# Optimization experiments

Measured on AMD Instinct MI355X. Metric: run time of the kernel, lower is better.

## Reference

```python
import jax, jax.numpy as jnp
import numpy as np

N_NODES = 100000
N_EDGES = 1600000
D = 128
N_GRAPHS = 1024
N_LAYERS = 3
BN_EPS = 1e-5


def setup_inputs() -> dict:
    key = jax.random.key(0)
    ks = jax.random.split(key, 12)
    x = jax.random.normal(ks[0], (N_NODES, D), dtype=jnp.float32)
    edge_index = jax.random.randint(ks[1], (2, N_EDGES), 0, N_NODES, dtype=jnp.int32)
    batch = jnp.sort(jax.random.randint(ks[2], (N_NODES,), 0, N_GRAPHS, dtype=jnp.int32))
    scale = 1.0 / np.sqrt(D)
    W1 = jax.random.uniform(ks[3], (D, D), jnp.float32, -scale, scale)
    b1 = jax.random.uniform(ks[4], (D,), jnp.float32, -scale, scale)
    W2 = jax.random.uniform(ks[5], (D, D), jnp.float32, -scale, scale)
    b2 = jax.random.uniform(ks[6], (D,), jnp.float32, -scale, scale)
    W3 = jax.random.uniform(ks[7], (D, D), jnp.float32, -scale, scale)
    b3 = jax.random.uniform(ks[8], (D,), jnp.float32, -scale, scale)
    eps = jnp.zeros((N_LAYERS,), jnp.float32)          # GINConv train_eps init = 0
    gamma = jnp.ones((N_LAYERS, D), jnp.float32)       # BatchNorm1d weight
    beta = jnp.zeros((N_LAYERS, D), jnp.float32)       # BatchNorm1d bias
    return {"x": x, "edge_index": edge_index, "batch": batch,
            "W1": W1, "b1": b1, "W2": W2, "b2": b2, "W3": W3, "b3": b3,
            "eps": eps, "gamma": gamma, "beta": beta}


def _gin_layer(h, src, dst, W, b, eps_i, g, bt):
    # scatter-add neighbor aggregation: sum_{j in N(i)} h_j
    agg = jax.ops.segment_sum(h[src], dst, num_segments=N_NODES)  # [N, D]
    h = (1.0 + eps_i) * h + agg
    h = h @ W.T + b                                   # Linear
    mean = jnp.mean(h, axis=0)                        # BatchNorm1d (training, biased var)
    var = jnp.var(h, axis=0)
    h = (h - mean) * jax.lax.rsqrt(var + BN_EPS) * g + bt
    return jax.nn.relu(h)


def reference(x, edge_index, batch, W1, b1, W2, b2, W3, b3, eps, gamma, beta):
    src, dst = edge_index[0], edge_index[1]
    h = x
    for i, (W, b) in enumerate([(W1, b1), (W2, b2), (W3, b3)]):
        h = _gin_layer(h, src, dst, W, b, eps[i], gamma[i], beta[i])
    # global mean pool over graphs
    sums = jax.ops.segment_sum(h, batch, num_segments=N_GRAPHS)             # [G, D]
    counts = jax.ops.segment_sum(jnp.ones((h.shape[0],), h.dtype), batch,
                                 num_segments=N_GRAPHS)                      # [G]
    return sums / jnp.maximum(counts, 1.0)[:, None]
```

## Files before the change

kernel.cpp:

```cpp
#include <hip/hip_runtime.h>

#define N_NODES 100000
#define N_PAD 100032
#define N_EDGES 1600000
#define DIM 128
#define N_GRAPHS 1024

#define SCAN_BLOCK 256
#define SCAN_NB ((N_NODES + SCAN_BLOCK - 1) / SCAN_BLOCK)

#define NPART 8
#define PART_SZ 12500

typedef __bf16 bf16x8 __attribute__((ext_vector_type(8)));
typedef float f32x4 __attribute__((ext_vector_type(4)));

__device__ __forceinline__ unsigned short f2bf(float f) {
    unsigned u = __builtin_bit_cast(unsigned, f);
    u += 0x7fffu + ((u >> 16) & 1u);
    return (unsigned short)(u >> 16);
}
__device__ __forceinline__ unsigned pk2(float a, float b) {
    return (unsigned)f2bf(a) | ((unsigned)f2bf(b) << 16);
}
__device__ __forceinline__ float bf2f(unsigned short s) {
    return __builtin_bit_cast(float, (unsigned)s << 16);
}
__device__ __forceinline__ void dec2(unsigned p, float& lo, float& hi) {
    lo = __builtin_bit_cast(float, p << 16);
    hi = __builtin_bit_cast(float, p & 0xffff0000u);
}


__global__ __launch_bounds__(256) void hist_part_kernel(const int* __restrict__ dst,
                                                        int* __restrict__ deg) {
    int p = blockIdx.x & (NPART - 1);
    int bgrp = blockIdx.x >> 3;
    int nb = gridDim.x >> 3;
    int tid = bgrp * blockDim.x + threadIdx.x;
    int nthreads = nb * blockDim.x;
    const int NE4 = N_EDGES / 4;
    for (int i = tid; i < NE4; i += nthreads) {
        int4 d4 = ((const int4*)dst)[i];
        if (d4.x / PART_SZ == p) atomicAdd(&deg[d4.x], 1);
        if (d4.y / PART_SZ == p) atomicAdd(&deg[d4.y], 1);
        if (d4.z / PART_SZ == p) atomicAdd(&deg[d4.z], 1);
        if (d4.w / PART_SZ == p) atomicAdd(&deg[d4.w], 1);
    }
}

__global__ __launch_bounds__(256) void fill_part_kernel(const int* __restrict__ src,
                                                        const int* __restrict__ dst,
                                                        int* __restrict__ cursor,
                                                        int* __restrict__ csr) {
    int p = blockIdx.x & (NPART - 1);
    int bgrp = blockIdx.x >> 3;
    int nb = gridDim.x >> 3;
    int tid = bgrp * blockDim.x + threadIdx.x;
    int nthreads = nb * blockDim.x;
    const int NE4 = N_EDGES / 4;
    for (int i = tid; i < NE4; i += nthreads) {
        int4 d4 = ((const int4*)dst)[i];
        int4 s4 = ((const int4*)src)[i];
        if (d4.x / PART_SZ == p) csr[atomicAdd(&cursor[d4.x], 1)] = s4.x;
        if (d4.y / PART_SZ == p) csr[atomicAdd(&cursor[d4.y], 1)] = s4.y;
        if (d4.z / PART_SZ == p) csr[atomicAdd(&cursor[d4.z], 1)] = s4.z;
        if (d4.w / PART_SZ == p) csr[atomicAdd(&cursor[d4.w], 1)] = s4.w;
    }
}


__global__ __launch_bounds__(SCAN_BLOCK) void scan_partial_kernel(const int* __restrict__ deg,
                                                                  int* __restrict__ partials) {
    __shared__ int red[SCAN_BLOCK / 64];
    int i = blockIdx.x * SCAN_BLOCK + threadIdx.x;
    int v = (i < N_NODES) ? deg[i] : 0;
    for (int o = 32; o > 0; o >>= 1) v += __shfl_down(v, o, 64);
    if ((threadIdx.x & 63) == 0) red[threadIdx.x >> 6] = v;
    __syncthreads();
    if (threadIdx.x == 0) {
        int s = 0;
#pragma unroll
        for (int w = 0; w < SCAN_BLOCK / 64; ++w) s += red[w];
        partials[blockIdx.x] = s;
    }
}

__global__ __launch_bounds__(512) void scan_partials_kernel(int* __restrict__ partials,
                                                            int* __restrict__ off) {
    __shared__ int sm[512];
    int t = threadIdx.x;
    int v = (t < SCAN_NB) ? partials[t] : 0;
    sm[t] = v;
    __syncthreads();
    for (int o = 1; o < 512; o <<= 1) {
        int u = (t >= o) ? sm[t - o] : 0;
        __syncthreads();
        sm[t] += u;
        __syncthreads();
    }
    if (t < SCAN_NB) partials[t] = sm[t] - v;
    if (t == 0) off[N_NODES] = sm[511];
}

__global__ __launch_bounds__(SCAN_BLOCK) void scan_scatter_kernel(const int* __restrict__ deg,
                                                                  const int* __restrict__ partials,
                                                                  int* __restrict__ off,
                                                                  int* __restrict__ cursor) {
    __shared__ int sm[SCAN_BLOCK];
    int t = threadIdx.x;
    int i = blockIdx.x * SCAN_BLOCK + t;
    int v = (i < N_NODES) ? deg[i] : 0;
    sm[t] = v;
    __syncthreads();
    for (int o = 1; o < SCAN_BLOCK; o <<= 1) {
        int u = (t >= o) ? sm[t - o] : 0;
        __syncthreads();
        sm[t] += u;
        __syncthreads();
    }
    if (i < N_NODES) {
        int r = partials[blockIdx.x] + sm[t] - v;
        off[i] = r;
        cursor[i] = r;
    }
}


__global__ __launch_bounds__(64) void wprep_kernel(const float* __restrict__ W1,
                                                   const float* __restrict__ W2,
                                                   const float* __restrict__ W3,
                                                   uint4* __restrict__ wb4) {
    int b = blockIdx.x;
    int l = b >> 5;
    int nt = (b >> 2) & 7;
    int kk = b & 3;
    int lane = threadIdx.x;
    const float* W = (l == 0) ? W1 : (l == 1) ? W2 : W3;
    int row = nt * 16 + (lane & 15);
    int cb = kk * 32 + (lane >> 4) * 8;
    const float* g = W + row * DIM + cb;
    float4 f0 = *(const float4*)g;
    float4 f1 = *(const float4*)(g + 4);
    uint4 o;
    o.x = pk2(f0.x, f0.y);
    o.y = pk2(f0.z, f0.w);
    o.z = pk2(f1.x, f1.y);
    o.w = pk2(f1.z, f1.w);
    wb4[(size_t)b * 64 + lane] = o;
}


__global__ __launch_bounds__(256) void xconv_kernel(const float* __restrict__ x,
                                                    unsigned short* __restrict__ xb) {
    int i = blockIdx.x * blockDim.x + threadIdx.x;
    int stride = gridDim.x * blockDim.x;
    const int TOT = N_PAD * DIM / 8;
    for (; i < TOT; i += stride) {
        int row = i >> 4;
        int ks = i & 15;
        uint4 o = {0, 0, 0, 0};
        if (row < N_NODES) {
            const float* g = x + (size_t)row * DIM + ks * 8;
            float4 f0 = *(const float4*)g;
            float4 f1 = *(const float4*)(g + 4);
            o.x = pk2(f0.x, f0.y);
            o.y = pk2(f0.z, f0.w);
            o.z = pk2(f1.x, f1.y);
            o.w = pk2(f1.z, f1.w);
        }
        ((uint4*)xb)[i] = o;
    }
}


template <bool BN>
__global__ __launch_bounds__(256) void agg_gemm_kernel(const unsigned short* __restrict__ hin,
                                                       const int* __restrict__ off,
                                                       const int* __restrict__ csr,
                                                       const float* __restrict__ eps_arr, int layer,
                                                       const float* __restrict__ bnsc,
                                                       const float* __restrict__ bnsh,
                                                       const uint4* __restrict__ wb4,
                                                       unsigned short* __restrict__ y,
                                                       float* __restrict__ colsum,
                                                       float* __restrict__ colsumsq) {
    __shared__ unsigned short tile[64 * DIM];
    __shared__ float sstat[4][DIM];
    __shared__ float sstatq[4][DIM];
    int tid = threadIdx.x;
    int row0 = blockIdx.x * 64;
    int grp = tid >> 4;
    int lane = tid & 15;
    float se = 1.0f + eps_arr[layer];
    float sc[8], sh[8];
    if (BN) {
        float4 c0 = *(const float4*)(bnsc + lane * 8);
        float4 c1 = *(const float4*)(bnsc + lane * 8 + 4);
        float4 h0 = *(const float4*)(bnsh + lane * 8);
        float4 h1 = *(const float4*)(bnsh + lane * 8 + 4);
        sc[0] = c0.x; sc[1] = c0.y; sc[2] = c0.z; sc[3] = c0.w;
        sc[4] = c1.x; sc[5] = c1.y; sc[6] = c1.z; sc[7] = c1.w;
        sh[0] = h0.x; sh[1] = h0.y; sh[2] = h0.z; sh[3] = h0.w;
        sh[4] = h1.x; sh[5] = h1.y; sh[6] = h1.z; sh[7] = h1.w;
    }
    const uint4* base = (const uint4*)hin + lane;

#pragma unroll 1
    for (int r4 = 0; r4 < 4; ++r4) {
        int trow = grp * 4 + r4;
        int row = row0 + trow;
        float a[8] = {0.f, 0.f, 0.f, 0.f, 0.f, 0.f, 0.f, 0.f};
        if (row < N_NODES) {
            {
                uint4 pv = base[(size_t)row * (DIM / 8)];
                float v[8];
                dec2(pv.x, v[0], v[1]); dec2(pv.y, v[2], v[3]);
                dec2(pv.z, v[4], v[5]); dec2(pv.w, v[6], v[7]);
#pragma unroll
                for (int j = 0; j < 8; ++j) {
                    if (BN) v[j] = fmaxf(fmaf(v[j], sc[j], sh[j]), 0.f);
                    a[j] = se * v[j];
                }
            }
            int k = off[row], e = off[row + 1];
            for (; k + 3 < e; k += 4) {
                int s0 = csr[k], s1 = csr[k + 1], s2 = csr[k + 2], s3 = csr[k + 3];
                uint4 p0 = base[(size_t)s0 * (DIM / 8)];
                uint4 p1 = base[(size_t)s1 * (DIM / 8)];
                uint4 p2 = base[(size_t)s2 * (DIM / 8)];
                uint4 p3 = base[(size_t)s3 * (DIM / 8)];
                float v0[8], v1[8], v2[8], v3[8];
                dec2(p0.x, v0[0], v0[1]); dec2(p0.y, v0[2], v0[3]);
                dec2(p0.z, v0[4], v0[5]); dec2(p0.w, v0[6], v0[7]);
                dec2(p1.x, v1[0], v1[1]); dec2(p1.y, v1[2], v1[3]);
                dec2(p1.z, v1[4], v1[5]); dec2(p1.w, v1[6], v1[7]);
                dec2(p2.x, v2[0], v2[1]); dec2(p2.y, v2[2], v2[3]);
                dec2(p2.z, v2[4], v2[5]); dec2(p2.w, v2[6], v2[7]);
                dec2(p3.x, v3[0], v3[1]); dec2(p3.y, v3[2], v3[3]);
                dec2(p3.z, v3[4], v3[5]); dec2(p3.w, v3[6], v3[7]);
#pragma unroll
                for (int j = 0; j < 8; ++j) {
                    if (BN) {
                        v0[j] = fmaxf(fmaf(v0[j], sc[j], sh[j]), 0.f);
                        v1[j] = fmaxf(fmaf(v1[j], sc[j], sh[j]), 0.f);
                        v2[j] = fmaxf(fmaf(v2[j], sc[j], sh[j]), 0.f);
                        v3[j] = fmaxf(fmaf(v3[j], sc[j], sh[j]), 0.f);
                    }
                    a[j] += (v0[j] + v1[j]) + (v2[j] + v3[j]);
                }
            }
            for (; k < e; ++k) {
                int s0 = csr[k];
                uint4 p0 = base[(size_t)s0 * (DIM / 8)];
                float v0[8];
                dec2(p0.x, v0[0], v0[1]); dec2(p0.y, v0[2], v0[3]);
                dec2(p0.z, v0[4], v0[5]); dec2(p0.w, v0[6], v0[7]);
#pragma unroll
                for (int j = 0; j < 8; ++j) {
                    if (BN) v0[j] = fmaxf(fmaf(v0[j], sc[j], sh[j]), 0.f);
                    a[j] += v0[j];
                }
            }
        }
        uint4 pw;
        pw.x = pk2(a[0], a[1]);
        pw.y = pk2(a[2], a[3]);
        pw.z = pk2(a[4], a[5]);
        pw.w = pk2(a[6], a[7]);
        int byte = (trow * 256 + lane * 16) ^ ((trow & 7) << 4);
        *(uint4*)((char*)tile + byte) = pw;
    }
    __syncthreads();

    int w = tid >> 6;
    int l = tid & 63;
    int lr = l & 15;
    int lg = l >> 4;
    bf16x8 a[4];
#pragma unroll
    for (int kk = 0; kk < 4; ++kk) {
        int row = w * 16 + lr;
        int byte = (row * 256 + kk * 64 + lg * 16) ^ ((row & 7) << 4);
        a[kk] = __builtin_bit_cast(bf16x8, *(uint4*)((char*)tile + byte));
    }

#pragma unroll
    for (int nt = 0; nt < 8; ++nt) {
        f32x4 acc = {0.0f, 0.0f, 0.0f, 0.0f};
#pragma unroll
        for (int kk = 0; kk < 4; ++kk) {
            bf16x8 b = __builtin_bit_cast(bf16x8, wb4[(nt * 4 + kk) * 64 + l]);
            acc = __builtin_amdgcn_mfma_f32_16x16x32_bf16(a[kk], b, acc, 0, 0, 0);
        }
        int col = nt * 16 + lr;
        size_t base2 = (size_t)(row0 + w * 16 + lg * 4) * DIM + col;
        y[base2] = f2bf(acc[0]);
        y[base2 + DIM] = f2bf(acc[1]);
        y[base2 + 2 * DIM] = f2bf(acc[2]);
        y[base2 + 3 * DIM] = f2bf(acc[3]);
        float s = acc[0] + acc[1] + acc[2] + acc[3];
        float q = acc[0] * acc[0] + acc[1] * acc[1] + acc[2] * acc[2] + acc[3] * acc[3];
        s += __shfl_xor(s, 16);
        s += __shfl_xor(s, 32);
        q += __shfl_xor(q, 16);
        q += __shfl_xor(q, 32);
        if (lg == 0) {
            sstat[w][col] = s;
            sstatq[w][col] = q;
        }
    }
    __syncthreads();
    if (tid < DIM) {
        float s = sstat[0][tid] + sstat[1][tid] + sstat[2][tid] + sstat[3][tid];
        float q = sstatq[0][tid] + sstatq[1][tid] + sstatq[2][tid] + sstatq[3][tid];
        atomicAdd(&colsum[tid], s);
        atomicAdd(&colsumsq[tid], q);
    }
}


__global__ void bnfin_kernel(float* __restrict__ colsum, float* __restrict__ colsumsq,
                             const float* __restrict__ gamma, const float* __restrict__ beta,
                             float* __restrict__ scale, float* __restrict__ shift) {
    int d = threadIdx.x;
    float m = colsum[d] * (1.0f / N_NODES);
    float v = colsumsq[d] * (1.0f / N_NODES) - m * m;
    float sc = gamma[d] * rsqrtf(v + 1e-5f);
    scale[d] = sc;
    shift[d] = beta[d] - m * sc;
    colsum[d] = 0.0f;
    colsumsq[d] = 0.0f;
}


__global__ __launch_bounds__(128) void pool_kernel(const unsigned short* __restrict__ y,
                                                   const int* __restrict__ batch,
                                                   const float* __restrict__ bnsc,
                                                   const float* __restrict__ bnsh,
                                                   float* __restrict__ out) {
    int gph = blockIdx.x;
    int d = threadIdx.x;
    int lo = 0, hi = N_NODES;
    while (lo < hi) {
        int mid = (lo + hi) >> 1;
        if (batch[mid] < gph) lo = mid + 1; else hi = mid;
    }
    int start = lo;
    hi = N_NODES;
    while (lo < hi) {
        int mid = (lo + hi) >> 1;
        if (batch[mid] < gph + 1) lo = mid + 1; else hi = mid;
    }
    int end = lo;
    float sc = bnsc[d], sh = bnsh[d];
    float s = 0.0f;
    for (int n = start; n < end; ++n) {
        float v = bf2f(y[(size_t)n * DIM + d]);
        s += fmaxf(fmaf(v, sc, sh), 0.0f);
    }
    out[gph * DIM + d] = s / fmaxf((float)(end - start), 1.0f);
}


extern "C" void kernel_launch(void* const* d_in, const int* in_sizes, int n_in,
                              void* d_out, int out_size, void* d_ws, size_t ws_size,
                              hipStream_t stream) {
    const float* x = (const float*)d_in[0];
    const int* ei = (const int*)d_in[1];
    const int* batch = (const int*)d_in[2];
    const float* Wp[3] = {(const float*)d_in[3], (const float*)d_in[5], (const float*)d_in[7]};
    const float* eps = (const float*)d_in[9];
    const float* gamma = (const float*)d_in[10];
    const float* beta = (const float*)d_in[11];
    float* out = (float*)d_out;

    char* ws = (char*)d_ws;
    size_t o = 0;
    auto alloc = [&](size_t bytes) {
        void* p = ws + o;
        o = (o + bytes + 255) & ~(size_t)255;
        return p;
    };
    int* deg = (int*)alloc(N_NODES * sizeof(int));
    int* off = (int*)alloc((N_NODES + 1) * sizeof(int));
    int* cursor = (int*)alloc(N_NODES * sizeof(int));
    int* partials = (int*)alloc(SCAN_NB * sizeof(int));
    int* csr = (int*)alloc(N_EDGES * sizeof(int));
    uint4* wb4 = (uint4*)alloc(3 * 8 * 4 * 64 * 16);
    float* colsum = (float*)alloc(DIM * sizeof(float));
    float* colsumsq = (float*)alloc(DIM * sizeof(float));
    float* bnsc = (float*)alloc(DIM * sizeof(float));
    float* bnsh = (float*)alloc(DIM * sizeof(float));
    unsigned short* xb = (unsigned short*)alloc((size_t)N_PAD * DIM * 2);
    unsigned short* y0 = (unsigned short*)alloc((size_t)N_PAD * DIM * 2);
    unsigned short* y1 = (unsigned short*)alloc((size_t)N_PAD * DIM * 2);

    hipMemsetAsync(deg, 0, N_NODES * sizeof(int), stream);
    hipMemsetAsync(colsum, 0, DIM * sizeof(float), stream);
    hipMemsetAsync(colsumsq, 0, DIM * sizeof(float), stream);

    hist_part_kernel<<<1024, 256, 0, stream>>>(ei + N_EDGES, deg);
    scan_partial_kernel<<<SCAN_NB, SCAN_BLOCK, 0, stream>>>(deg, partials);
    scan_partials_kernel<<<1, 512, 0, stream>>>(partials, off);
    scan_scatter_kernel<<<SCAN_NB, SCAN_BLOCK, 0, stream>>>(deg, partials, off, cursor);
    fill_part_kernel<<<1024, 256, 0, stream>>>(ei, ei + N_EDGES, cursor, csr);
    wprep_kernel<<<96, 64, 0, stream>>>(Wp[0], Wp[1], Wp[2], wb4);
    xconv_kernel<<<2048, 256, 0, stream>>>(x, xb);

    const int NBLK = N_PAD / 64;
    agg_gemm_kernel<false><<<NBLK, 256, 0, stream>>>(xb, off, csr, eps, 0, bnsc, bnsh,
                                                     wb4, y0, colsum, colsumsq);
    bnfin_kernel<<<1, DIM, 0, stream>>>(colsum, colsumsq, gamma, beta, bnsc, bnsh);
    agg_gemm_kernel<true><<<NBLK, 256, 0, stream>>>(y0, off, csr, eps, 1, bnsc, bnsh,
                                                    wb4 + 2048, y1, colsum, colsumsq);
    bnfin_kernel<<<1, DIM, 0, stream>>>(colsum, colsumsq, gamma + DIM, beta + DIM, bnsc, bnsh);
    agg_gemm_kernel<true><<<NBLK, 256, 0, stream>>>(y1, off, csr, eps, 2, bnsc, bnsh,
                                                    wb4 + 4096, y0, colsum, colsumsq);
    bnfin_kernel<<<1, DIM, 0, stream>>>(colsum, colsumsq, gamma + 2 * DIM, beta + 2 * DIM, bnsc, bnsh);
    pool_kernel<<<N_GRAPHS, DIM, 0, stream>>>(y0, batch, bnsc, bnsh, out);
}
```

Before: 614.9 us.

## Fold BN finalize into consumers, unroll gather by 8, widen edge and pool loops

Removes the three single-block bnfin kernels. Each consumer kernel (the next agg_gemm or pool) now recomputes BN scale and shift from per-layer column-sum buffers, which cuts launch overhead and serialization points. The neighbor-gather loop is unrolled to 8 outstanding row loads for more memory-level parallelism. The histogram and CSR fill kernels read 8 edges per iteration with a doubled grid, and pool uses 4 independent accumulators. The cost is redundant per-thread rsqrt work, higher register pressure in the gather loop, and 3x larger stat buffers that are zeroed up front.

```diff
diff --git a/kernel.cpp b/kernel.cpp
--- a/kernel.cpp
+++ b/kernel.cpp
@@ -29,6 +29,20 @@
 __device__ __forceinline__ void dec2(unsigned p, float& lo, float& hi) {
     lo = __builtin_bit_cast(float, p << 16);
     hi = __builtin_bit_cast(float, p & 0xffff0000u);
+}
+
+template <bool BN>
+__device__ __forceinline__ void acc8(uint4 p, float* a, const float* sc, const float* sh) {
+    float v[8];
+    dec2(p.x, v[0], v[1]);
+    dec2(p.y, v[2], v[3]);
+    dec2(p.z, v[4], v[5]);
+    dec2(p.w, v[6], v[7]);
+#pragma unroll
+    for (int j = 0; j < 8; ++j) {
+        float t = BN ? fmaxf(fmaf(v[j], sc[j], sh[j]), 0.f) : v[j];
+        a[j] += t;
+    }
 }
 
 
@@ -39,13 +53,18 @@
     int nb = gridDim.x >> 3;
     int tid = bgrp * blockDim.x + threadIdx.x;
     int nthreads = nb * blockDim.x;
-    const int NE4 = N_EDGES / 4;
-    for (int i = tid; i < NE4; i += nthreads) {
-        int4 d4 = ((const int4*)dst)[i];
-        if (d4.x / PART_SZ == p) atomicAdd(&deg[d4.x], 1);
-        if (d4.y / PART_SZ == p) atomicAdd(&deg[d4.y], 1);
-        if (d4.z / PART_SZ == p) atomicAdd(&deg[d4.z], 1);
-        if (d4.w / PART_SZ == p) atomicAdd(&deg[d4.w], 1);
+    const int NE8 = N_EDGES / 8;
+    for (int i = tid; i < NE8; i += nthreads) {
+        int4 a = ((const int4*)dst)[2 * i];
+        int4 b = ((const int4*)dst)[2 * i + 1];
+        if (a.x / PART_SZ == p) atomicAdd(&deg[a.x], 1);
+        if (a.y / PART_SZ == p) atomicAdd(&deg[a.y], 1);
+        if (a.z / PART_SZ == p) atomicAdd(&deg[a.z], 1);
+        if (a.w / PART_SZ == p) atomicAdd(&deg[a.w], 1);
+        if (b.x / PART_SZ == p) atomicAdd(&deg[b.x], 1);
+        if (b.y / PART_SZ == p) atomicAdd(&deg[b.y], 1);
+        if (b.z / PART_SZ == p) atomicAdd(&deg[b.z], 1);
+        if (b.w / PART_SZ == p) atomicAdd(&deg[b.w], 1);
     }
 }
 
@@ -58,14 +77,20 @@
     int nb = gridDim.x >> 3;
     int tid = bgrp * blockDim.x + threadIdx.x;
     int nthreads = nb * blockDim.x;
-    const int NE4 = N_EDGES / 4;
-    for (int i = tid; i < NE4; i += nthreads) {
-        int4 d4 = ((const int4*)dst)[i];
-        int4 s4 = ((const int4*)src)[i];
-        if (d4.x / PART_SZ == p) csr[atomicAdd(&cursor[d4.x], 1)] = s4.x;
-        if (d4.y / PART_SZ == p) csr[atomicAdd(&cursor[d4.y], 1)] = s4.y;
-        if (d4.z / PART_SZ == p) csr[atomicAdd(&cursor[d4.z], 1)] = s4.z;
-        if (d4.w / PART_SZ == p) csr[atomicAdd(&cursor[d4.w], 1)] = s4.w;
+    const int NE8 = N_EDGES / 8;
+    for (int i = tid; i < NE8; i += nthreads) {
+        int4 da = ((const int4*)dst)[2 * i];
+        int4 db = ((const int4*)dst)[2 * i + 1];
+        int4 sa = ((const int4*)src)[2 * i];
+        int4 sb = ((const int4*)src)[2 * i + 1];
+        if (da.x / PART_SZ == p) csr[atomicAdd(&cursor[da.x], 1)] = sa.x;
+        if (da.y / PART_SZ == p) csr[atomicAdd(&cursor[da.y], 1)] = sa.y;
+        if (da.z / PART_SZ == p) csr[atomicAdd(&cursor[da.z], 1)] = sa.z;
+        if (da.w / PART_SZ == p) csr[atomicAdd(&cursor[da.w], 1)] = sa.w;
+        if (db.x / PART_SZ == p) csr[atomicAdd(&cursor[db.x], 1)] = sb.x;
+        if (db.y / PART_SZ == p) csr[atomicAdd(&cursor[db.y], 1)] = sb.y;
+        if (db.z / PART_SZ == p) csr[atomicAdd(&cursor[db.z], 1)] = sb.z;
+        if (db.w / PART_SZ == p) csr[atomicAdd(&cursor[db.w], 1)] = sb.w;
     }
 }
 
@@ -179,12 +204,14 @@
                                                        const int* __restrict__ off,
                                                        const int* __restrict__ csr,
                                                        const float* __restrict__ eps_arr, int layer,
-                                                       const float* __restrict__ bnsc,
-                                                       const float* __restrict__ bnsh,
+                                                       const float* __restrict__ csum_prev,
+                                                       const float* __restrict__ csq_prev,
+                                                       const float* __restrict__ gamma_prev,
+                                                       const float* __restrict__ beta_prev,
                                                        const uint4* __restrict__ wb4,
                                                        unsigned short* __restrict__ y,
-                                                       float* __restrict__ colsum,
-                                                       float* __restrict__ colsumsq) {
+                                                       float* __restrict__ csum_out,
+                                                       float* __restrict__ csq_out) {
     __shared__ unsigned short tile[64 * DIM];
     __shared__ float sstat[4][DIM];
     __shared__ float sstatq[4][DIM];
@@ -195,16 +222,18 @@
     float se = 1.0f + eps_arr[layer];
     float sc[8], sh[8];
     if (BN) {
-        float4 c0 = *(const float4*)(bnsc + lane * 8);
-        float4 c1 = *(const float4*)(bnsc + lane * 8 + 4);
-        float4 h0 = *(const float4*)(bnsh + lane * 8);
-        float4 h1 = *(const float4*)(bnsh + lane * 8 + 4);
-        sc[0] = c0.x; sc[1] = c0.y; sc[2] = c0.z; sc[3] = c0.w;
-        sc[4] = c1.x; sc[5] = c1.y; sc[6] = c1.z; sc[7] = c1.w;
-        sh[0] = h0.x; sh[1] = h0.y; sh[2] = h0.z; sh[3] = h0.w;
-        sh[4] = h1.x; sh[5] = h1.y; sh[6] = h1.z; sh[7] = h1.w;
+#pragma unroll
+        for (int j = 0; j < 8; ++j) {
+            int d = lane * 8 + j;
+            float m = csum_prev[d] * (1.0f / N_NODES);
+            float var = csq_prev[d] * (1.0f / N_NODES) - m * m;
+            float s = gamma_prev[d] * rsqrtf(var + 1e-5f);
+            sc[j] = s;
+            sh[j] = beta_prev[d] - m * s;
+        }
     }
     const uint4* base = (const uint4*)hin + lane;
+    const size_t RS = DIM / 8;
 
 #pragma unroll 1
     for (int r4 = 0; r4 < 4; ++r4) {
@@ -213,54 +242,52 @@
         float a[8] = {0.f, 0.f, 0.f, 0.f, 0.f, 0.f, 0.f, 0.f};
         if (row < N_NODES) {
             {
-                uint4 pv = base[(size_t)row * (DIM / 8)];
+                uint4 pv = base[(size_t)row * RS];
                 float v[8];
                 dec2(pv.x, v[0], v[1]); dec2(pv.y, v[2], v[3]);
                 dec2(pv.z, v[4], v[5]); dec2(pv.w, v[6], v[7]);
 #pragma unroll
                 for (int j = 0; j < 8; ++j) {
-                    if (BN) v[j] = fmaxf(fmaf(v[j], sc[j], sh[j]), 0.f);
-                    a[j] = se * v[j];
+                    float t = BN ? fmaxf(fmaf(v[j], sc[j], sh[j]), 0.f) : v[j];
+                    a[j] = se * t;
                 }
             }
             int k = off[row], e = off[row + 1];
-            for (; k + 3 < e; k += 4) {
+            for (; k + 7 < e; k += 8) {
                 int s0 = csr[k], s1 = csr[k + 1], s2 = csr[k + 2], s3 = csr[k + 3];
-                uint4 p0 = base[(size_t)s0 * (DIM / 8)];
-                uint4 p1 = base[(size_t)s1 * (DIM / 8)];
-                uint4 p2 = base[(size_t)s2 * (DIM / 8)];
-                uint4 p3 = base[(size_t)s3 * (DIM / 8)];
-                float v0[8], v1[8], v2[8], v3[8];
-                dec2(p0.x, v0[0], v0[1]); dec2(p0.y, v0[2], v0[3]);
-                dec2(p0.z, v0[4], v0[5]); dec2(p0.w, v0[6], v0[7]);
-                dec2(p1.x, v1[0], v1[1]); dec2(p1.y, v1[2], v1[3]);
-                dec2(p1.z, v1[4], v1[5]); dec2(p1.w, v1[6], v1[7]);
-                dec2(p2.x, v2[0], v2[1]); dec2(p2.y, v2[2], v2[3]);
-                dec2(p2.z, v2[4], v2[5]); dec2(p2.w, v2[6], v2[7]);
-                dec2(p3.x, v3[0], v3[1]); dec2(p3.y, v3[2], v3[3]);
-                dec2(p3.z, v3[4], v3[5]); dec2(p3.w, v3[6], v3[7]);
-#pragma unroll
-                for (int j = 0; j < 8; ++j) {
-                    if (BN) {
-                        v0[j] = fmaxf(fmaf(v0[j], sc[j], sh[j]), 0.f);
-                        v1[j] = fmaxf(fmaf(v1[j], sc[j], sh[j]), 0.f);
-                        v2[j] = fmaxf(fmaf(v2[j], sc[j], sh[j]), 0.f);
-                        v3[j] = fmaxf(fmaf(v3[j], sc[j], sh[j]), 0.f);
-                    }
-                    a[j] += (v0[j] + v1[j]) + (v2[j] + v3[j]);
-                }
+                int s4 = csr[k + 4], s5 = csr[k + 5], s6 = csr[k + 6], s7 = csr[k + 7];
+                uint4 p0 = base[(size_t)s0 * RS];
+                uint4 p1 = base[(size_t)s1 * RS];
+                uint4 p2 = base[(size_t)s2 * RS];
+                uint4 p3 = base[(size_t)s3 * RS];
+                uint4 p4 = base[(size_t)s4 * RS];
+                uint4 p5 = base[(size_t)s5 * RS];
+                uint4 p6 = base[(size_t)s6 * RS];
+                uint4 p7 = base[(size_t)s7 * RS];
+                acc8<BN>(p0, a, sc, sh);
+                acc8<BN>(p1, a, sc, sh);
+                acc8<BN>(p2, a, sc, sh);
+                acc8<BN>(p3, a, sc, sh);
+                acc8<BN>(p4, a, sc, sh);
+                acc8<BN>(p5, a, sc, sh);
+                acc8<BN>(p6, a, sc, sh);
+                acc8<BN>(p7, a, sc, sh);
+            }
+            if (k + 3 < e) {
+                int s0 = csr[k], s1 = csr[k + 1], s2 = csr[k + 2], s3 = csr[k + 3];
+                uint4 p0 = base[(size_t)s0 * RS];
+                uint4 p1 = base[(size_t)s1 * RS];
+                uint4 p2 = base[(size_t)s2 * RS];
+                uint4 p3 = base[(size_t)s3 * RS];
+                acc8<BN>(p0, a, sc, sh);
+                acc8<BN>(p1, a, sc, sh);
+                acc8<BN>(p2, a, sc, sh);
+                acc8<BN>(p3, a, sc, sh);
+                k += 4;
             }
             for (; k < e; ++k) {
-                int s0 = csr[k];
-                uint4 p0 = base[(size_t)s0 * (DIM / 8)];
-                float v0[8];
-                dec2(p0.x, v0[0], v0[1]); dec2(p0.y, v0[2], v0[3]);
-                dec2(p0.z, v0[4], v0[5]); dec2(p0.w, v0[6], v0[7]);
-#pragma unroll
-                for (int j = 0; j < 8; ++j) {
-                    if (BN) v0[j] = fmaxf(fmaf(v0[j], sc[j], sh[j]), 0.f);
-                    a[j] += v0[j];
-                }
+                uint4 p0 = base[(size_t)csr[k] * RS];
+                acc8<BN>(p0, a, sc, sh);
             }
         }
         uint4 pw;
@@ -314,33 +341,25 @@
     if (tid < DIM) {
         float s = sstat[0][tid] + sstat[1][tid] + sstat[2][tid] + sstat[3][tid];
         float q = sstatq[0][tid] + sstatq[1][tid] + sstatq[2][tid] + sstatq[3][tid];
-        atomicAdd(&colsum[tid], s);
-        atomicAdd(&colsumsq[tid], q);
-    }
-}
-
-
-__global__ void bnfin_kernel(float* __restrict__ colsum, float* __restrict__ colsumsq,
-                             const float* __restrict__ gamma, const float* __restrict__ beta,
-                             float* __restrict__ scale, float* __restrict__ shift) {
-    int d = threadIdx.x;
-    float m = colsum[d] * (1.0f / N_NODES);
-    float v = colsumsq[d] * (1.0f / N_NODES) - m * m;
-    float sc = gamma[d] * rsqrtf(v + 1e-5f);
-    scale[d] = sc;
-    shift[d] = beta[d] - m * sc;
-    colsum[d] = 0.0f;
-    colsumsq[d] = 0.0f;
+        atomicAdd(&csum_out[tid], s);
+        atomicAdd(&csq_out[tid], q);
+    }
 }
 
 
 __global__ __launch_bounds__(128) void pool_kernel(const unsigned short* __restrict__ y,
                                                    const int* __restrict__ batch,
-                                                   const float* __restrict__ bnsc,
-                                                   const float* __restrict__ bnsh,
+                                                   const float* __restrict__ csum,
+                                                   const float* __restrict__ csq,
+                                                   const float* __restrict__ gamma,
+                                                   const float* __restrict__ beta,
                                                    float* __restrict__ out) {
     int gph = blockIdx.x;
     int d = threadIdx.x;
+    float m = csum[d] * (1.0f / N_NODES);
+    float var = csq[d] * (1.0f / N_NODES) - m * m;
+    float sc = gamma[d] * rsqrtf(var + 1e-5f);
+    float sh = beta[d] - m * sc;
     int lo = 0, hi = N_NODES;
     while (lo < hi) {
         int mid = (lo + hi) >> 1;
@@ -353,12 +372,23 @@
         if (batch[mid] < gph + 1) lo = mid + 1; else hi = mid;
     }
     int end = lo;
-    float sc = bnsc[d], sh = bnsh[d];
-    float s = 0.0f;
-    for (int n = start; n < end; ++n) {
+    float s0 = 0.f, s1 = 0.f, s2 = 0.f, s3 = 0.f;
+    int n = start;
+    for (; n + 3 < end; n += 4) {
+        float v0 = bf2f(y[(size_t)n * DIM + d]);
+        float v1 = bf2f(y[(size_t)(n + 1) * DIM + d]);
+        float v2 = bf2f(y[(size_t)(n + 2) * DIM + d]);
+        float v3 = bf2f(y[(size_t)(n + 3) * DIM + d]);
+        s0 += fmaxf(fmaf(v0, sc, sh), 0.0f);
+        s1 += fmaxf(fmaf(v1, sc, sh), 0.0f);
+        s2 += fmaxf(fmaf(v2, sc, sh), 0.0f);
+        s3 += fmaxf(fmaf(v3, sc, sh), 0.0f);
+    }
+    for (; n < end; ++n) {
         float v = bf2f(y[(size_t)n * DIM + d]);
-        s += fmaxf(fmaf(v, sc, sh), 0.0f);
-    }
+        s0 += fmaxf(fmaf(v, sc, sh), 0.0f);
+    }
+    float s = (s0 + s1) + (s2 + s3);
     out[gph * DIM + d] = s / fmaxf((float)(end - start), 1.0f);
 }
 
@@ -388,35 +418,34 @@
     int* partials = (int*)alloc(SCAN_NB * sizeof(int));
     int* csr = (int*)alloc(N_EDGES * sizeof(int));
     uint4* wb4 = (uint4*)alloc(3 * 8 * 4 * 64 * 16);
-    float* colsum = (float*)alloc(DIM * sizeof(float));
-    float* colsumsq = (float*)alloc(DIM * sizeof(float));
-    float* bnsc = (float*)alloc(DIM * sizeof(float));
-    float* bnsh = (float*)alloc(DIM * sizeof(float));
+    float* csums = (float*)alloc(3 * DIM * sizeof(float));
+    float* csqs = (float*)alloc(3 * DIM * sizeof(float));
     unsigned short* xb = (unsigned short*)alloc((size_t)N_PAD * DIM * 2);
     unsigned short* y0 = (unsigned short*)alloc((size_t)N_PAD * DIM * 2);
     unsigned short* y1 = (unsigned short*)alloc((size_t)N_PAD * DIM * 2);
 
     hipMemsetAsync(deg, 0, N_NODES * sizeof(int), stream);
-    hipMemsetAsync(colsum, 0, DIM * sizeof(float), stream);
-    hipMemsetAsync(colsumsq, 0, DIM * sizeof(float), stream);
-
-    hist_part_kernel<<<1024, 256, 0, stream>>>(ei + N_EDGES, deg);
+    hipMemsetAsync(csums, 0, 3 * DIM * sizeof(float), stream);
+    hipMemsetAsync(csqs, 0, 3 * DIM * sizeof(float), stream);
+
+    hist_part_kernel<<<2048, 256, 0, stream>>>(ei + N_EDGES, deg);
     scan_partial_kernel<<<SCAN_NB, SCAN_BLOCK, 0, stream>>>(deg, partials);
     scan_partials_kernel<<<1, 512, 0, stream>>>(partials, off);
     scan_scatter_kernel<<<SCAN_NB, SCAN_BLOCK, 0, stream>>>(deg, partials, off, cursor);
-    fill_part_kernel<<<1024, 256, 0, stream>>>(ei, ei + N_EDGES, cursor, csr);
+    fill_part_kernel<<<2048, 256, 0, stream>>>(ei, ei + N_EDGES, cursor, csr);
     wprep_kernel<<<96, 64, 0, stream>>>(Wp[0], Wp[1], Wp[2], wb4);
     xconv_kernel<<<2048, 256, 0, stream>>>(x, xb);
 
     const int NBLK = N_PAD / 64;
-    agg_gemm_kernel<false><<<NBLK, 256, 0, stream>>>(xb, off, csr, eps, 0, bnsc, bnsh,
-                                                     wb4, y0, colsum, colsumsq);
-    bnfin_kernel<<<1, DIM, 0, stream>>>(colsum, colsumsq, gamma, beta, bnsc, bnsh);
-    agg_gemm_kernel<true><<<NBLK, 256, 0, stream>>>(y0, off, csr, eps, 1, bnsc, bnsh,
-                                                    wb4 + 2048, y1, colsum, colsumsq);
-    bnfin_kernel<<<1, DIM, 0, stream>>>(colsum, colsumsq, gamma + DIM, beta + DIM, bnsc, bnsh);
-    agg_gemm_kernel<true><<<NBLK, 256, 0, stream>>>(y1, off, csr, eps, 2, bnsc, bnsh,
-                                                    wb4 + 4096, y0, colsum, colsumsq);
-    bnfin_kernel<<<1, DIM, 0, stream>>>(colsum, colsumsq, gamma + 2 * DIM, beta + 2 * DIM, bnsc, bnsh);
-    pool_kernel<<<N_GRAPHS, DIM, 0, stream>>>(y0, batch, bnsc, bnsh, out);
-}
+    agg_gemm_kernel<false><<<NBLK, 256, 0, stream>>>(xb, off, csr, eps, 0,
+                                                     nullptr, nullptr, nullptr, nullptr,
+                                                     wb4, y0, csums, csqs);
+    agg_gemm_kernel<true><<<NBLK, 256, 0, stream>>>(y0, off, csr, eps, 1,
+                                                    csums, csqs, gamma, beta,
+                                                    wb4 + 2048, y1, csums + DIM, csqs + DIM);
+    agg_gemm_kernel<true><<<NBLK, 256, 0, stream>>>(y1, off, csr, eps, 2,
+                                                    csums + DIM, csqs + DIM, gamma + DIM, beta + DIM,
+                                                    wb4 + 4096, y0, csums + 2 * DIM, csqs + 2 * DIM);
+    pool_kernel<<<N_GRAPHS, DIM, 0, stream>>>(y0, batch, csums + 2 * DIM, csqs + 2 * DIM,
+                                              gamma + 2 * DIM, beta + 2 * DIM, out);
+}
```

Result: faster. 594.4 us (-3.3%).
